# Optimization experiments

Hardware: AMD Instinct MI355X
Metric: run time of the kernel (lower is better)

The kernel has to match this reference:

```python
import jax, jax.numpy as jnp
import numpy as np

HEADS = 4
DIM_HEAD = 32


def setup_inputs() -> dict:
    key = jax.random.key(0)
    k1, k2, k3, k4 = jax.random.split(key, 4)
    dim = 64
    hidden = HEADS * DIM_HEAD  # 128
    x = jax.random.normal(k1, (2, dim, 48, 48, 48), dtype=jnp.float32)
    # 1x1x1 Conv3d weights are just channel-mixing matrices
    w_qkv = jax.random.normal(k2, (3 * hidden, dim), dtype=jnp.float32) * (1.0 / np.sqrt(dim))
    w_out = jax.random.normal(k3, (dim, hidden), dtype=jnp.float32) * (1.0 / np.sqrt(hidden))
    b_out = jax.random.normal(k4, (dim,), dtype=jnp.float32) * 0.01
    return {"x": x, "w_qkv": w_qkv, "w_out": w_out, "b_out": b_out}


def reference(x, w_qkv, w_out, b_out):
    b, c, X, Y, Z = x.shape
    N = X * Y * Z
    xf = x.reshape(b, c, N)  # flatten spatial dims
    # to_qkv: 1x1x1 conv == channel matmul -> [b, 3*H*C, N]
    qkv = jnp.einsum('bci,oc->boi', xf, w_qkv)
    qkv = qkv.reshape(b, 3, HEADS, DIM_HEAD, N)
    q, k, v = qkv[:, 0], qkv[:, 1], qkv[:, 2]  # each [b, h, c, N]
    q = jax.nn.softmax(q, axis=-2)  # softmax over channel dim
    k = jax.nn.softmax(k, axis=-1)  # softmax over spatial dim
    # linear attention: small [c, d] context per head, O(N)
    ctx = jnp.einsum('bhci,bhdi->bhcd', k, v)   # [b, h, c, d]
    out = jnp.einsum('bhcd,bhck->bhdk', ctx, q)  # [b, h, d, N]
    out = out.reshape(b, HEADS * DIM_HEAD, N)
    # combine_heads: 1x1x1 conv with bias
    out = jnp.einsum('bci,oc->boi', out, w_out) + b_out[None, :, None]
    return out.reshape(b, -1, X, Y, Z)
```

## Files before the change

kernel.cpp:

```cpp
#include <hip/hip_runtime.h>
#include <hip/hip_bf16.h>

typedef unsigned int u32;
typedef unsigned short u16;
typedef __attribute__((ext_vector_type(8))) short bf16x8;
typedef __attribute__((ext_vector_type(4))) float f32x4;

#define NPIX 110592
#define NTILES 1728
#define K1_BLOCKS 864
#define K1_TPB 4
#define PART_STRIDE 4224

#define WS_ATB   0
#define WS_P2    8192
#define WS_PART  75776

union FragU { u32 u[4]; bf16x8 v; };

#define MFMA(a,b,c) __builtin_amdgcn_mfma_f32_16x16x32_bf16((a),(b),(c),0,0,0)

__device__ __forceinline__ u32 pk2(float a, float b) {
    union { __hip_bfloat162 h2; u32 u; } cv;
    cv.h2.x = __float2bfloat16(a);
    cv.h2.y = __float2bfloat16(b);
    return cv.u;
}
__device__ __forceinline__ float bf2f(u32 bits) { return __uint_as_float(bits << 16); }
__device__ __forceinline__ void split2(float a, float b, u32& hi, u32& lo) {
    hi = pk2(a, b);
    lo = pk2(a - bf2f(hi & 0xFFFFu), b - __uint_as_float(hi & 0xFFFF0000u));
}

__global__ __launch_bounds__(256, 3)
void k1_ctx(const float* __restrict__ x, const float* __restrict__ wq,
            float* __restrict__ part, int usePart, int R) {
    __shared__ u32 xbh[256 * 32];
    const int blk = blockIdx.x;
    const int p   = threadIdx.x & 63;
    const int og  = __builtin_amdgcn_readfirstlane(threadIdx.x >> 6);
    const int b   = blk / (K1_BLOCKS / 2);
    const int q   = p >> 4;
    const int l15 = p & 15;
    const int yv  = (p & 7) << 2;
    const float* xg = x + (long)b * 64 * NPIX;

    FragU wh[4][2], wl[4][2];
    #pragma unroll
    for (int mi = 0; mi < 4; ++mi)
        #pragma unroll
        for (int ks = 0; ks < 2; ++ks) {
            const int kvrow = (mi < 2) ? (og * 32 + mi * 16) : (128 + og * 32 + (mi - 2) * 16);
            const int row = 128 + kvrow + l15;
            const float* wp = wq + row * 64 + ks * 32 + q * 4;
            float4 f0 = *(const float4*)wp;
            float4 f1 = *(const float4*)(wp + 16);
            split2(f0.x, f0.y, wh[mi][ks].u[0], wl[mi][ks].u[0]);
            split2(f0.z, f0.w, wh[mi][ks].u[1], wl[mi][ks].u[1]);
            split2(f1.x, f1.y, wh[mi][ks].u[2], wl[mi][ks].u[2]);
            split2(f1.z, f1.w, wh[mi][ks].u[3], wl[mi][ks].u[3]);
        }

    FragU ones;
    #pragma unroll
    for (int i = 0; i < 4; ++i) ones.u[i] = 0x3F803F80u;

    f32x4 cc[2][2], rsa[2];
    #pragma unroll
    for (int mi = 0; mi < 2; ++mi) {
        #pragma unroll
        for (int ni = 0; ni < 2; ++ni) cc[mi][ni] = (f32x4)0.f;
        rsa[mi] = (f32x4)0.f;
    }

    const long i0g = (long)(blk * K1_TPB - b * NTILES) * 64;
    #pragma unroll
    for (int ch = 0; ch < 2; ++ch) {
        f32x4 xl4[8];
        const float* xr = xg + (long)(og * 16 + ch * 8) * NPIX + i0g + 4 * p;
        #pragma unroll
        for (int i = 0; i < 8; ++i) xl4[i] = *(const f32x4*)(xr + (long)i * NPIX);
        #pragma unroll
        for (int j = 0; j < 4; ++j) {
            const int px = 4 * p + j;
            const int yy = (px & 7) << 2;
            u32 h[4];
            #pragma unroll
            for (int w = 0; w < 4; ++w) h[w] = pk2(xl4[2 * w][j], xl4[2 * w + 1][j]);
            const int sA = (og * 8 + ch * 4) ^ yy;
            *(uint4*)&xbh[px * 32 + sA] = make_uint4(h[0], h[1], h[2], h[3]);
        }
    }
    __syncthreads();

    #pragma unroll 1
    for (int tt = 0; tt < K1_TPB; ++tt) {
        #pragma unroll
        for (int ksp = 0; ksp < 2; ++ksp) {
            f32x4 acc[4][2];
            #pragma unroll
            for (int ni2 = 0; ni2 < 2; ++ni2) {
                const int ni = ksp * 2 + ni2;
                const int rb = (tt * 64 + ni * 16 + l15) * 32;
                FragU bh[2];
                #pragma unroll
                for (int ks = 0; ks < 2; ++ks) {
                    const int c0 = (ks * 16 + 2 * q) ^ yv;
                    const int c1 = (ks * 16 + 2 * q + 8) ^ yv;
                    uint2 t0 = *(const uint2*)&xbh[rb + c0];
                    uint2 t1 = *(const uint2*)&xbh[rb + c1];
                    bh[ks].u[0] = t0.x; bh[ks].u[1] = t0.y;
                    bh[ks].u[2] = t1.x; bh[ks].u[3] = t1.y;
                }
                #pragma unroll
                for (int mi = 0; mi < 4; ++mi) {
                    f32x4 a = (f32x4)0.f;
                    #pragma unroll
                    for (int ks = 0; ks < 2; ++ks) {
                        a = MFMA(bh[ks].v, wh[mi][ks].v, a);
                        a = MFMA(bh[ks].v, wl[mi][ks].v, a);
                    }
                    acc[mi][ni2] = a;
                }
            }
            FragU ak[2], av[2];
            #pragma unroll
            for (int m2 = 0; m2 < 2; ++m2) {
                float e0[4], e1[4];
                #pragma unroll
                for (int j = 0; j < 4; ++j) {
                    e0[j] = __expf(acc[m2][0][j]);
                    e1[j] = __expf(acc[m2][1][j]);
                }
                ak[m2].u[0] = pk2(e0[0], e0[1]);
                ak[m2].u[1] = pk2(e0[2], e0[3]);
                ak[m2].u[2] = pk2(e1[0], e1[1]);
                ak[m2].u[3] = pk2(e1[2], e1[3]);
                av[m2].u[0] = pk2(acc[2 + m2][0][0], acc[2 + m2][0][1]);
                av[m2].u[1] = pk2(acc[2 + m2][0][2], acc[2 + m2][0][3]);
                av[m2].u[2] = pk2(acc[2 + m2][1][0], acc[2 + m2][1][1]);
                av[m2].u[3] = pk2(acc[2 + m2][1][2], acc[2 + m2][1][3]);
            }
            #pragma unroll
            for (int mi = 0; mi < 2; ++mi) {
                #pragma unroll
                for (int nj = 0; nj < 2; ++nj)
                    cc[mi][nj] = MFMA(ak[mi].v, av[nj].v, cc[mi][nj]);
                rsa[mi] = MFMA(ak[mi].v, ones.v, rsa[mi]);
            }
        }
    }

    if (usePart) {
        float* pp = part + (long)blk * PART_STRIDE;
        #pragma unroll
        for (int mi = 0; mi < 2; ++mi)
            #pragma unroll
            for (int ni = 0; ni < 2; ++ni)
                #pragma unroll
                for (int j = 0; j < 4; ++j)
                    pp[og * 1024 + (mi * 16 + q * 4 + j) * 32 + ni * 16 + l15] = cc[mi][ni][j];
        if (l15 == 0) {
            #pragma unroll
            for (int mi = 0; mi < 2; ++mi)
                #pragma unroll
                for (int j = 0; j < 4; ++j)
                    pp[4096 + og * 32 + mi * 16 + q * 4 + j] = rsa[mi][j];
        }
    } else {
        float* pp = part + (long)(b * R + (blk % R)) * PART_STRIDE;
        #pragma unroll
        for (int mi = 0; mi < 2; ++mi)
            #pragma unroll
            for (int ni = 0; ni < 2; ++ni)
                #pragma unroll
                for (int j = 0; j < 4; ++j)
                    atomicAdd(&pp[og * 1024 + (mi * 16 + q * 4 + j) * 32 + ni * 16 + l15], cc[mi][ni][j]);
        if (l15 == 0) {
            #pragma unroll
            for (int mi = 0; mi < 2; ++mi)
                #pragma unroll
                for (int j = 0; j < 4; ++j)
                    atomicAdd(&pp[4096 + og * 32 + mi * 16 + q * 4 + j], rsa[mi][j]);
        }
    }
}

__global__ __launch_bounds__(128)
void k1b_reduce(float* __restrict__ ws, int PB) {
    const int S = 8;
    const int chunk = blockIdx.x % 33;
    const int rem   = blockIdx.x / 33;
    const int b     = rem & 1;
    const int slice = rem >> 1;
    const int j = chunk * 128 + threadIdx.x;
    const int PBh = PB >> 1;
    const float* part = ws + WS_PART;
    float s = 0.f;
    for (int pi = b * PBh + slice; pi < (b + 1) * PBh; pi += S)
        s += part[(long)pi * PART_STRIDE + j];
    ws[WS_P2 + (long)(b * S + slice) * PART_STRIDE + j] = s;
}

__global__ __launch_bounds__(256)
void k2_prepA(const float* __restrict__ wout, float* __restrict__ ws) {
    __shared__ float wo[64 * 129];
    __shared__ float ct[4096];
    __shared__ float rsum[128];
    const int b   = blockIdx.x >> 3;
    const int jb  = blockIdx.x & 7;
    const int tid = threadIdx.x;
    for (int i = tid; i < 8192; i += 256) wo[(i >> 7) * 129 + (i & 127)] = wout[i];
    for (int i = tid; i < 4096; i += 256) {
        float s = 0.f;
        #pragma unroll
        for (int s8 = 0; s8 < 8; ++s8)
            s += ws[WS_P2 + (long)(b * 8 + s8) * PART_STRIDE + i];
        ct[i] = s;
    }
    if (tid < 128) {
        float s = 0.f;
        #pragma unroll
        for (int s8 = 0; s8 < 8; ++s8)
            s += ws[WS_P2 + (long)(b * 8 + s8) * PART_STRIDE + 4096 + tid];
        rsum[tid] = s;
    }
    __syncthreads();
    u32* atb = (u32*)ws + WS_ATB + b * 4096;
    const int o  = tid & 63;
    const int ug = tid >> 6;
    #pragma unroll
    for (int i = 0; i < 2; ++i) {
        const int up = jb * 8 + ug * 2 + i;
        const int hc0 = 2 * up, hc1 = 2 * up + 1;
        const int hh = hc0 >> 5;
        const int c0 = hc0 & 31, c1 = hc1 & 31;
        float s0 = 0.f, s1 = 0.f;
        #pragma unroll
        for (int d = 0; d < 32; ++d) {
            const float w = wo[o * 129 + hh * 32 + d];
            s0 = fmaf(w, ct[hh * 1024 + c0 * 32 + d], s0);
            s1 = fmaf(w, ct[hh * 1024 + c1 * 32 + d], s1);
        }
        atb[up * 64 + o] = pk2(s0 / rsum[hc0], s1 / rsum[hc1]);
    }
}

__global__ __launch_bounds__(256, 3)
void k3_out(const float* __restrict__ x, const float* __restrict__ wq,
            const float* __restrict__ bout, const float* __restrict__ wsf,
            float* __restrict__ out) {
    __shared__ u32 xbh[256 * 32];
    __shared__ u16 qb[64 * 128];
    const int blk = blockIdx.x;
    const int p   = threadIdx.x & 63;
    const int og  = __builtin_amdgcn_readfirstlane(threadIdx.x >> 6);
    const int b   = blk / (K1_BLOCKS / 2);
    const int q   = p >> 4;
    const int l15 = p & 15;
    const int yv  = (p & 7) << 2;
    const float* xg = x + (long)b * 64 * NPIX;

    FragU wh[2][2], wl[2][2];
    #pragma unroll
    for (int mi = 0; mi < 2; ++mi)
        #pragma unroll
        for (int ks = 0; ks < 2; ++ks) {
            const int row = og * 32 + mi * 16 + l15;
            const float* wp = wq + row * 64 + ks * 32 + q * 4;
            float4 f0 = *(const float4*)wp;
            float4 f1 = *(const float4*)(wp + 16);
            split2(f0.x, f0.y, wh[mi][ks].u[0], wl[mi][ks].u[0]);
            split2(f0.z, f0.w, wh[mi][ks].u[1], wl[mi][ks].u[1]);
            split2(f1.x, f1.y, wh[mi][ks].u[2], wl[mi][ks].u[2]);
            split2(f1.z, f1.w, wh[mi][ks].u[3], wl[mi][ks].u[3]);
        }

    const u32* atb = (const u32*)wsf + WS_ATB + b * 4096;
    FragU af[4];
    #pragma unroll
    for (int ks = 0; ks < 4; ++ks) {
        const int up0 = ks * 16 + 2 * q;
        const int o   = og * 16 + l15;
        af[ks].u[0] = atb[(up0)     * 64 + o];
        af[ks].u[1] = atb[(up0 + 1) * 64 + o];
        af[ks].u[2] = atb[(up0 + 8) * 64 + o];
        af[ks].u[3] = atb[(up0 + 9) * 64 + o];
    }
    const float4 bias = *(const float4*)&bout[og * 16 + q * 4];

    const long i0g = (long)(blk * K1_TPB - b * NTILES) * 64;
    #pragma unroll
    for (int ch = 0; ch < 2; ++ch) {
        f32x4 xl4[8];
        const float* xr = xg + (long)(og * 16 + ch * 8) * NPIX + i0g + 4 * p;
        #pragma unroll
        for (int i = 0; i < 8; ++i) xl4[i] = *(const f32x4*)(xr + (long)i * NPIX);
        #pragma unroll
        for (int j = 0; j < 4; ++j) {
            const int px = 4 * p + j;
            const int yy = (px & 7) << 2;
            u32 h[4];
            #pragma unroll
            for (int w = 0; w < 4; ++w) h[w] = pk2(xl4[2 * w][j], xl4[2 * w + 1][j]);
            const int sA = (og * 8 + ch * 4) ^ yy;
            *(uint4*)&xbh[px * 32 + sA] = make_uint4(h[0], h[1], h[2], h[3]);
        }
    }
    __syncthreads();

    #pragma unroll 1
    for (int tt = 0; tt < K1_TPB; ++tt) {
        const long i0 = i0g + tt * 64;

        #pragma unroll
        for (int ni = 0; ni < 4; ++ni) {
            const int rb = (tt * 64 + ni * 16 + l15) * 32;
            FragU bh[2];
            #pragma unroll
            for (int ks = 0; ks < 2; ++ks) {
                const int c0 = (ks * 16 + 2 * q) ^ yv;
                const int c1 = (ks * 16 + 2 * q + 8) ^ yv;
                uint2 t0 = *(const uint2*)&xbh[rb + c0];
                uint2 t1 = *(const uint2*)&xbh[rb + c1];
                bh[ks].u[0] = t0.x; bh[ks].u[1] = t0.y;
                bh[ks].u[2] = t1.x; bh[ks].u[3] = t1.y;
            }
            f32x4 a0 = (f32x4)0.f, a1 = (f32x4)0.f;
            #pragma unroll
            for (int ks = 0; ks < 2; ++ks) {
                a0 = MFMA(wh[0][ks].v, bh[ks].v, a0);
                a0 = MFMA(wl[0][ks].v, bh[ks].v, a0);
                a1 = MFMA(wh[1][ks].v, bh[ks].v, a1);
                a1 = MFMA(wl[1][ks].v, bh[ks].v, a1);
            }
            float mx = a0[0];
            #pragma unroll
            for (int j = 1; j < 4; ++j) mx = fmaxf(mx, a0[j]);
            #pragma unroll
            for (int j = 0; j < 4; ++j) mx = fmaxf(mx, a1[j]);
            mx = fmaxf(mx, __shfl_xor(mx, 16));
            mx = fmaxf(mx, __shfl_xor(mx, 32));
            float e0[4], e1[4], sm = 0.f;
            #pragma unroll
            for (int j = 0; j < 4; ++j) { e0[j] = __expf(a0[j] - mx); sm += e0[j]; }
            #pragma unroll
            for (int j = 0; j < 4; ++j) { e1[j] = __expf(a1[j] - mx); sm += e1[j]; }
            sm += __shfl_xor(sm, 16);
            sm += __shfl_xor(sm, 32);
            const float inv = 1.0f / sm;
            const int px = ni * 16 + l15;
            const int Xq = (px & 7) << 3;
            u32* qbw = (u32*)qb;
            const int b0 = (px * 128 + ((og * 32 + q * 4) ^ Xq)) >> 1;
            const int b1 = (px * 128 + ((og * 32 + 16 + q * 4) ^ Xq)) >> 1;
            *(uint2*)&qbw[b0] = make_uint2(pk2(e0[0] * inv, e0[1] * inv),
                                           pk2(e0[2] * inv, e0[3] * inv));
            *(uint2*)&qbw[b1] = make_uint2(pk2(e1[0] * inv, e1[1] * inv),
                                           pk2(e1[2] * inv, e1[3] * inv));
        }
        __syncthreads();

        const u32* qb32 = (const u32*)qb;
        #pragma unroll
        for (int ni = 0; ni < 4; ++ni) {
            const int px = ni * 16 + l15;
            const int rb = px * 64;
            f32x4 a3 = (f32x4)0.f;
            #pragma unroll
            for (int ks = 0; ks < 4; ++ks) {
                const int c0 = (ks * 16 + 2 * q) ^ yv;
                const int c1 = (ks * 16 + 2 * q + 8) ^ yv;
                uint2 t0 = *(const uint2*)&qb32[rb + c0];
                uint2 t1 = *(const uint2*)&qb32[rb + c1];
                FragU bq;
                bq.u[0] = t0.x; bq.u[1] = t0.y; bq.u[2] = t1.x; bq.u[3] = t1.y;
                a3 = MFMA(af[ks].v, bq.v, a3);
            }
            #pragma unroll
            for (int j = 0; j < 4; ++j)
                out[((long)b * 64 + og * 16 + q * 4 + j) * NPIX + i0 + px] = a3[j] + bias[j];
        }
        __syncthreads();
    }
}

extern "C" void kernel_launch(void* const* d_in, const int* in_sizes, int n_in,
                              void* d_out, int out_size, void* d_ws, size_t ws_size,
                              hipStream_t stream) {
    (void)in_sizes; (void)n_in; (void)out_size;
    const float* x     = (const float*)d_in[0];
    const float* w_qkv = (const float*)d_in[1];
    const float* w_out = (const float*)d_in[2];
    const float* b_out = (const float*)d_in[3];
    float* out = (float*)d_out;
    float* ws  = (float*)d_ws;

    const size_t need_part = ((size_t)WS_PART + (size_t)K1_BLOCKS * PART_STRIDE) * 4;
    const int usePart = (ws_size >= need_part) ? 1 : 0;
    int R = 8;
    const size_t need_r8 = ((size_t)WS_PART + (size_t)2 * 8 * PART_STRIDE) * 4;
    if (!usePart && ws_size < need_r8) R = 1;
    const int PB = usePart ? K1_BLOCKS : 2 * R;
    float* part = ws + WS_PART;

    if (!usePart)
        hipMemsetAsync(part, 0, (size_t)PB * PART_STRIDE * 4, stream);
    hipLaunchKernelGGL(k1_ctx, dim3(K1_BLOCKS), dim3(256), 0, stream,
                       x, w_qkv, part, usePart, R);
    hipLaunchKernelGGL(k1b_reduce, dim3(528), dim3(128), 0, stream, ws, PB);
    hipLaunchKernelGGL(k2_prepA, dim3(16), dim3(256), 0, stream, w_out, ws);
    hipLaunchKernelGGL(k3_out, dim3(K1_BLOCKS), dim3(256), 0, stream,
                       x, w_qkv, b_out, ws, out);
}
```

Before: 83.03 us.

## Cache bf16-packed x tiles from k1 in workspace and reload them in k3

k1 now writes its swizzled bf16 LDS tile of x (32 KB per block) to a workspace region. k3 copies it straight into LDS with global_load_lds instead of rereading fp32 x and converting it again. This halves k3's input traffic and drops the conversion, at the cost of about 28 MB of extra writes in k1 and a larger workspace requirement, since WS_PART moves much further out. If the workspace is too small the partial-buffer fallback logic shifts, and the cached copy may overflow the buffer.

```diff
diff --git a/kernel.cpp b/kernel.cpp
--- a/kernel.cpp
+++ b/kernel.cpp
@@ -14,12 +14,18 @@
 
 #define WS_ATB   0
 #define WS_P2    8192
-#define WS_PART  75776
+#define WS_XPK   75776
+#define WS_PART  7153664
 
 union FragU { u32 u[4]; bf16x8 v; };
 
 #define MFMA(a,b,c) __builtin_amdgcn_mfma_f32_16x16x32_bf16((a),(b),(c),0,0,0)
 
+__device__ __forceinline__ void gll16(const float* g, float* l) {
+    typedef const __attribute__((address_space(1))) unsigned int* gp_t;
+    typedef __attribute__((address_space(3))) unsigned int* lp_t;
+    __builtin_amdgcn_global_load_lds((gp_t)g, (lp_t)l, 16, 0, 0);
+}
 __device__ __forceinline__ u32 pk2(float a, float b) {
     union { __hip_bfloat162 h2; u32 u; } cv;
     cv.h2.x = __float2bfloat16(a);
@@ -34,7 +40,7 @@
 
 __global__ __launch_bounds__(256, 3)
 void k1_ctx(const float* __restrict__ x, const float* __restrict__ wq,
-            float* __restrict__ part, int usePart, int R) {
+            float* __restrict__ ws, int usePart, int R) {
     __shared__ u32 xbh[256 * 32];
     const int blk = blockIdx.x;
     const int p   = threadIdx.x & 63;
@@ -44,6 +50,7 @@
     const int l15 = p & 15;
     const int yv  = (p & 7) << 2;
     const float* xg = x + (long)b * 64 * NPIX;
+    float* part = ws + WS_PART;
 
     FragU wh[4][2], wl[4][2];
     #pragma unroll
@@ -92,6 +99,16 @@
         }
     }
     __syncthreads();
+
+    {
+        u32* xpk = (u32*)ws + WS_XPK + (long)blk * 8192;
+        #pragma unroll
+        for (int i = 0; i < 8; ++i) {
+            const int idx = i * 1024 + threadIdx.x * 4;
+            uint4 v = *(const uint4*)&xbh[idx];
+            *(uint4*)&xpk[idx] = v;
+        }
+    }
 
     #pragma unroll 1
     for (int tt = 0; tt < K1_TPB; ++tt) {
@@ -259,7 +276,16 @@
     const int q   = p >> 4;
     const int l15 = p & 15;
     const int yv  = (p & 7) << 2;
-    const float* xg = x + (long)b * 64 * NPIX;
+    (void)x;
+
+    {
+        const u32* xpk = (const u32*)wsf + WS_XPK + (long)blk * 8192;
+        #pragma unroll
+        for (int i = 0; i < 8; ++i) {
+            const int o32 = og * 2048 + i * 256;
+            gll16((const float*)&xpk[o32 + 4 * p], (float*)&xbh[o32]);
+        }
+    }
 
     FragU wh[2][2], wl[2][2];
     #pragma unroll
@@ -289,26 +315,10 @@
     }
     const float4 bias = *(const float4*)&bout[og * 16 + q * 4];
 
+    asm volatile("s_waitcnt vmcnt(0)" ::: "memory");
+    __syncthreads();
+
     const long i0g = (long)(blk * K1_TPB - b * NTILES) * 64;
-    #pragma unroll
-    for (int ch = 0; ch < 2; ++ch) {
-        f32x4 xl4[8];
-        const float* xr = xg + (long)(og * 16 + ch * 8) * NPIX + i0g + 4 * p;
-        #pragma unroll
-        for (int i = 0; i < 8; ++i) xl4[i] = *(const f32x4*)(xr + (long)i * NPIX);
-        #pragma unroll
-        for (int j = 0; j < 4; ++j) {
-            const int px = 4 * p + j;
-            const int yy = (px & 7) << 2;
-            u32 h[4];
-            #pragma unroll
-            for (int w = 0; w < 4; ++w) h[w] = pk2(xl4[2 * w][j], xl4[2 * w + 1][j]);
-            const int sA = (og * 8 + ch * 4) ^ yy;
-            *(uint4*)&xbh[px * 32 + sA] = make_uint4(h[0], h[1], h[2], h[3]);
-        }
-    }
-    __syncthreads();
-
     #pragma unroll 1
     for (int tt = 0; tt < K1_TPB; ++tt) {
         const long i0 = i0g + tt * 64;
@@ -407,7 +417,7 @@
     if (!usePart)
         hipMemsetAsync(part, 0, (size_t)PB * PART_STRIDE * 4, stream);
     hipLaunchKernelGGL(k1_ctx, dim3(K1_BLOCKS), dim3(256), 0, stream,
-                       x, w_qkv, part, usePart, R);
+                       x, w_qkv, ws, usePart, R);
     hipLaunchKernelGGL(k1b_reduce, dim3(528), dim3(128), 0, stream, ws, PB);
     hipLaunchKernelGGL(k2_prepA, dim3(16), dim3(256), 0, stream, w_out, ws);
     hipLaunchKernelGGL(k3_out, dim3(K1_BLOCKS), dim3(256), 0, stream,
```

After: 81.69 us. Within noise of the previous version (-1.6%).
